# Kernel tuning notes

Hardware: AMD Instinct MI355X
Metric: run time of the kernel (lower is better)

## Reference

```python
import jax, jax.numpy as jnp
import numpy as np

M, K, N = 32, 8192, 8192      # tokens, infeatures, outfeatures
GROUP = 128                   # quantization group size along K
PACK = 8                      # 32 bits / 4 bits per value


def _dequant(qweight, scales):
    """Unpack int4 nibbles (packed 8-per-int32 along K) and apply per-group
    symmetric dequant: w = (q - 8) * scale, matching Marlin's fused dequant."""
    kp, n = qweight.shape  # (K//8, N)
    shifts = (4 * jnp.arange(PACK, dtype=jnp.int32))[None, :, None]
    q = ((qweight[:, None, :] >> shifts) & 15)          # (K//8, 8, N)
    q = q.reshape(kp * PACK, n).astype(jnp.float32)     # (K, N)
    groups = scales.shape[0]
    gsz = (kp * PACK) // groups
    w = (q.reshape(groups, gsz, n) - 8.0) * scales[:, None, :]
    return w.reshape(kp * PACK, n)                      # (K, N) fp


def setup_inputs() -> dict:
    key = jax.random.key(0)
    kA, kQ, kS, kB = jax.random.split(key, 4)
    A = jax.random.normal(kA, (M, K), jnp.float32)
    # draw raw 4-bit codes then pack 8 of them into each int32 along K
    q4 = jax.random.randint(kQ, (K, N), 0, 16, jnp.int32)
    shifts = (4 * jnp.arange(PACK, dtype=jnp.int32))[None, :, None]
    qweight = jnp.sum(q4.reshape(K // PACK, PACK, N) << shifts, axis=1).astype(jnp.int32)
    scales = jax.random.uniform(kS, (K // GROUP, N), jnp.float32, 0.005, 0.02)
    bias = jax.random.normal(kB, (N,), jnp.float32) * 0.01
    return {"A": A, "qweight": qweight, "scales": scales, "bias": bias}


def reference(A, qweight, scales, bias):
    # Marlin mul(A, B, C, s) computes C = A @ dequant(B, s); then + bias
    W = _dequant(qweight, scales)          # (K, N)
    return A @ W + bias                    # (M, N)
```

## Files before the change

### kernel.cpp

```cpp
#include <hip/hip_runtime.h>
#include <hip/hip_bf16.h>
#include <stdint.h>

#define M_DIM 32
#define K_DIM 8192
#define N_DIM 8192
#define NGROUPS 64
#define GSZ 128
#define KSPLIT 8
#define KPART (K_DIM / KSPLIT)
#define GPART (NGROUPS / KSPLIT)
#define BN 64

typedef __attribute__((ext_vector_type(8))) short short8;
typedef __attribute__((ext_vector_type(4))) float floatx4;

__global__ void marlin_prep_kernel(const float* __restrict__ A,
                                   uint16_t* __restrict__ Abf,
                                   float* __restrict__ R,
                                   float4* __restrict__ out4) {
    const int m = blockIdx.x;
    const int qtr = blockIdx.y;
    const int t = threadIdx.x;
    const int octet = qtr * 256 + t;
    const int k0 = octet * 8;

    {
        const int gtid = (qtr * 32 + m) * 256 + t;
        const float4 z = make_float4(0.f, 0.f, 0.f, 0.f);
        out4[gtid * 2] = z;
        out4[gtid * 2 + 1] = z;
    }

    const float* a = A + m * K_DIM + k0;
    uint16_t b[8];
    float sum = 0.f;
#pragma unroll
    for (int j = 0; j < 8; j++) {
        union { __hip_bfloat16 h; uint16_t u; } cv;
        cv.h = __float2bfloat16(a[j]);
        b[j] = cv.u;
        sum += __bfloat162float(cv.h);
    }
    uint32_t w0 = (uint32_t)b[0] | ((uint32_t)b[4] << 16);
    uint32_t w1 = (uint32_t)b[1] | ((uint32_t)b[5] << 16);
    uint32_t w2 = (uint32_t)b[2] | ((uint32_t)b[6] << 16);
    uint32_t w3 = (uint32_t)b[3] | ((uint32_t)b[7] << 16);
    uint4 packed = make_uint4(w0, w1, w2, w3);
    *(uint4*)(Abf + (size_t)m * K_DIM + k0) = packed;

#pragma unroll
    for (int off = 1; off < 16; off <<= 1) sum += __shfl_xor(sum, off, 16);
    if ((t & 15) == 0) R[m * NGROUPS + qtr * 16 + (t >> 4)] = sum;
}

__global__ __launch_bounds__(512, 4) void
MarlinQuantLinear_68556267979256_kernel(const int* __restrict__ qw,
                                        const float* __restrict__ scales,
                                        const float* __restrict__ bias,
                                        const uint16_t* __restrict__ Abf,
                                        const float* __restrict__ R,
                                        float* __restrict__ out) {
    __shared__ float r_lds[32 * 9];

    const int bx = blockIdx.x;
    const int bz = blockIdx.y;
    const int nbase = bx * BN;
    const int kbase = bz * KPART;
    const int gbase = bz * GPART;

    const int tid = threadIdx.x;
    const int w = tid >> 6;
    const int lane = tid & 63;
    const int quad = lane >> 4;
    const int l16 = lane & 15;
    const int mtile = w & 1;
    const int ntile = w >> 1;
    const int ncol = nbase + ntile * 16 + l16;

    if (tid < 256) {
        const int mm = tid >> 3, gg = tid & 7;
        r_lds[mm * 9 + gg] = 136.0f * R[mm * NGROUPS + gbase + gg];
    }
    __syncthreads();

    const float* scol = scales + (size_t)gbase * N_DIM + ncol;
    float s[GPART];
#pragma unroll
    for (int g = 0; g < GPART; g++) s[g] = scol[g * N_DIM];

    const int* qcol = qw + (size_t)(kbase >> 3) * N_DIM + ncol;
    uint32_t qv[GPART][4];
#pragma unroll
    for (int g = 0; g < GPART; g++)
#pragma unroll
        for (int t = 0; t < 4; t++)
            qv[g][t] = (uint32_t)qcol[(g * 16 + t * 4 + quad) * N_DIM];

    const uint16_t* arow = Abf + (size_t)(mtile * 16 + l16) * K_DIM
                               + kbase + quad * 8;
    short8 a_cur[4];
#pragma unroll
    for (int t = 0; t < 4; t++)
        a_cur[t] = *(const short8*)(arow + t * 32);

    floatx4 C = {0.f, 0.f, 0.f, 0.f};

#pragma unroll
    for (int g = 0; g < GPART; g++) {
        short8 a_nxt[4];
        if (g + 1 < GPART) {
#pragma unroll
            for (int t = 0; t < 4; t++)
                a_nxt[t] = *(const short8*)(arow + (g + 1) * 128 + t * 32);
        }
        floatx4 accg = {0.f, 0.f, 0.f, 0.f};
#pragma unroll
        for (int t = 0; t < 4; t++) {
            const uint32_t q = qv[g][t];
            union { uint32_t u[4]; short8 v; } fb;
            fb.u[0] = ( q        & 0x000F000Fu) | 0x43004300u;
            fb.u[1] = ((q >> 4)  & 0x000F000Fu) | 0x43004300u;
            fb.u[2] = ((q >> 8)  & 0x000F000Fu) | 0x43004300u;
            fb.u[3] = ((q >> 12) & 0x000F000Fu) | 0x43004300u;
            accg = __builtin_amdgcn_mfma_f32_16x16x32_bf16(a_cur[t], fb.v, accg, 0, 0, 0);
        }
#pragma unroll
        for (int r = 0; r < 4; r++) {
            const float tval = accg[r] - r_lds[(mtile * 16 + quad * 4 + r) * 9 + g];
            C[r] = fmaf(s[g], tval, C[r]);
        }
        if (g + 1 < GPART) {
#pragma unroll
            for (int t = 0; t < 4; t++) a_cur[t] = a_nxt[t];
        }
    }

    const float bv = (bz == 0) ? bias[ncol] : 0.0f;
#pragma unroll
    for (int r = 0; r < 4; r++) {
        const int m = mtile * 16 + quad * 4 + r;
        atomicAdd(&out[(size_t)m * N_DIM + ncol], C[r] + bv);
    }
}

extern "C" void kernel_launch(void* const* d_in, const int* in_sizes, int n_in,
                              void* d_out, int out_size, void* d_ws, size_t ws_size,
                              hipStream_t stream) {
    const float* A      = (const float*)d_in[0];
    const int*   qw     = (const int*)d_in[1];
    const float* scales = (const float*)d_in[2];
    const float* bias   = (const float*)d_in[3];
    float* out = (float*)d_out;

    uint16_t* Abf = (uint16_t*)d_ws;
    float*    R   = (float*)((char*)d_ws + (size_t)M_DIM * K_DIM * 2);

    marlin_prep_kernel<<<dim3(M_DIM, 4), 256, 0, stream>>>(A, Abf, R, (float4*)out);
    MarlinQuantLinear_68556267979256_kernel<<<dim3(N_DIM / BN, KSPLIT), 512, 0, stream>>>(
        qw, scales, bias, Abf, R, out);
}
```

Before: 109.7 us.

## Stage qweight and activation tiles through double-buffered LDS with vectorized loads

Replaces per-thread strided scalar global loads of packed weights and per-warp repeated activation loads with cooperative vectorized loads into double-buffered shared memory. Each group's weight and A tiles are written to padded LDS buffers and read back for MFMA operands. This cuts redundant global traffic and register pressure from preloading all weights, at the cost of a __syncthreads per group and extra LDS traffic. Register prefetch of the next group overlaps global loads with compute.

```diff
diff --git a/kernel.cpp b/kernel.cpp
--- a/kernel.cpp
+++ b/kernel.cpp
@@ -6,11 +6,13 @@
 #define K_DIM 8192
 #define N_DIM 8192
 #define NGROUPS 64
-#define GSZ 128
 #define KSPLIT 8
 #define KPART (K_DIM / KSPLIT)
 #define GPART (NGROUPS / KSPLIT)
 #define BN 64
+
+#define QSTRIDE 72
+#define ASTRIDE 66
 
 typedef __attribute__((ext_vector_type(8))) short short8;
 typedef __attribute__((ext_vector_type(4))) float floatx4;
@@ -46,8 +48,7 @@
     uint32_t w1 = (uint32_t)b[1] | ((uint32_t)b[5] << 16);
     uint32_t w2 = (uint32_t)b[2] | ((uint32_t)b[6] << 16);
     uint32_t w3 = (uint32_t)b[3] | ((uint32_t)b[7] << 16);
-    uint4 packed = make_uint4(w0, w1, w2, w3);
-    *(uint4*)(Abf + (size_t)m * K_DIM + k0) = packed;
+    *(uint4*)(Abf + (size_t)m * K_DIM + k0) = make_uint4(w0, w1, w2, w3);
 
 #pragma unroll
     for (int off = 1; off < 16; off <<= 1) sum += __shfl_xor(sum, off, 16);
@@ -61,12 +62,13 @@
                                         const uint16_t* __restrict__ Abf,
                                         const float* __restrict__ R,
                                         float* __restrict__ out) {
-    __shared__ float r_lds[32 * 9];
+    __shared__ uint32_t qbuf[2][16 * QSTRIDE];
+    __shared__ uint32_t abuf[2][32 * ASTRIDE];
+    __shared__ float    r_lds[32 * 9];
 
     const int bx = blockIdx.x;
     const int bz = blockIdx.y;
     const int nbase = bx * BN;
-    const int kbase = bz * KPART;
     const int gbase = bz * GPART;
 
     const int tid = threadIdx.x;
@@ -82,58 +84,56 @@
         const int mm = tid >> 3, gg = tid & 7;
         r_lds[mm * 9 + gg] = 136.0f * R[mm * NGROUPS + gbase + gg];
     }
-    __syncthreads();
 
     const float* scol = scales + (size_t)gbase * N_DIM + ncol;
     float s[GPART];
 #pragma unroll
     for (int g = 0; g < GPART; g++) s[g] = scol[g * N_DIM];
 
-    const int* qcol = qw + (size_t)(kbase >> 3) * N_DIM + ncol;
-    uint32_t qv[GPART][4];
-#pragma unroll
-    for (int g = 0; g < GPART; g++)
-#pragma unroll
-        for (int t = 0; t < 4; t++)
-            qv[g][t] = (uint32_t)qcol[(g * 16 + t * 4 + quad) * N_DIM];
+    const int qr = tid >> 5;
+    const int qc = (tid & 31) * 2;
+    const int* qsrc = qw + ((size_t)(bz * 128 + qr) * N_DIM) + nbase + qc;
+    const int am = tid >> 4;
+    const int aseg = (tid & 15) * 4;
+    const uint32_t* Ad = (const uint32_t*)Abf;
+    const uint32_t* asrc = Ad + (size_t)am * (K_DIM / 2) + bz * (KPART / 2) + aseg;
 
-    const uint16_t* arow = Abf + (size_t)(mtile * 16 + l16) * K_DIM
-                               + kbase + quad * 8;
-    short8 a_cur[4];
-#pragma unroll
-    for (int t = 0; t < 4; t++)
-        a_cur[t] = *(const short8*)(arow + t * 32);
+    uint2 qst = *(const uint2*)(qsrc);
+    uint4 ast = *(const uint4*)(asrc);
 
     floatx4 C = {0.f, 0.f, 0.f, 0.f};
 
 #pragma unroll
     for (int g = 0; g < GPART; g++) {
-        short8 a_nxt[4];
+        uint2 qnx; uint4 anx;
         if (g + 1 < GPART) {
-#pragma unroll
-            for (int t = 0; t < 4; t++)
-                a_nxt[t] = *(const short8*)(arow + (g + 1) * 128 + t * 32);
+            qnx = *(const uint2*)(qsrc + (size_t)(g + 1) * 16 * N_DIM);
+            anx = *(const uint4*)(asrc + (g + 1) * 64);
         }
+        *(uint2*)&qbuf[g & 1][qr * QSTRIDE + qc] = qst;
+        *(uint4*)&abuf[g & 1][am * ASTRIDE + aseg] = ast;
+        __syncthreads();
+
         floatx4 accg = {0.f, 0.f, 0.f, 0.f};
 #pragma unroll
         for (int t = 0; t < 4; t++) {
-            const uint32_t q = qv[g][t];
+            const uint32_t q = qbuf[g & 1][(t * 4 + quad) * QSTRIDE + ntile * 16 + l16];
             union { uint32_t u[4]; short8 v; } fb;
             fb.u[0] = ( q        & 0x000F000Fu) | 0x43004300u;
             fb.u[1] = ((q >> 4)  & 0x000F000Fu) | 0x43004300u;
             fb.u[2] = ((q >> 8)  & 0x000F000Fu) | 0x43004300u;
             fb.u[3] = ((q >> 12) & 0x000F000Fu) | 0x43004300u;
-            accg = __builtin_amdgcn_mfma_f32_16x16x32_bf16(a_cur[t], fb.v, accg, 0, 0, 0);
+            const short8 fa =
+                *(const short8*)&abuf[g & 1][(mtile * 16 + l16) * ASTRIDE + t * 16 + quad * 4];
+            accg = __builtin_amdgcn_mfma_f32_16x16x32_bf16(fa, fb.v, accg, 0, 0, 0);
         }
 #pragma unroll
         for (int r = 0; r < 4; r++) {
             const float tval = accg[r] - r_lds[(mtile * 16 + quad * 4 + r) * 9 + g];
             C[r] = fmaf(s[g], tval, C[r]);
         }
-        if (g + 1 < GPART) {
-#pragma unroll
-            for (int t = 0; t < 4; t++) a_cur[t] = a_nxt[t];
-        }
+        qst = qnx;
+        ast = anx;
     }
 
     const float bv = (bz == 0) ? bias[ncol] : 0.0f;
```

Measured after the change: 91.21 us. 1.2x faster.
